# Optimization experiments

Hardware: AMD Instinct MI355X
Metric: run time of the kernel (lower is better)

Reference implementation:

```python
import jax, jax.numpy as jnp
import numpy as np

NUM_EMBEDDINGS = 1024
EMBEDDING_DIM = 64
COMMITMENT_COST = 0.25
N_TOKENS = 131072  # e.g. batch 128 of 32x32 latent grids, flattened


def setup_inputs() -> dict:
    key = jax.random.key(0)
    k1, k2 = jax.random.split(key)
    z_e = jax.random.normal(k1, (N_TOKENS, EMBEDDING_DIM), dtype=jnp.float32)
    # torch init: uniform_(-1/K, 1/K)
    lim = 1.0 / NUM_EMBEDDINGS
    embeddings = jax.random.uniform(
        k2, (NUM_EMBEDDINGS, EMBEDDING_DIM), dtype=jnp.float32,
        minval=-lim, maxval=lim)
    return {"z_e": z_e, "embeddings": embeddings}


def reference(z_e, embeddings):
    # Squared L2 distances via the expanded form: ||z||^2 - 2 z.E^T + ||e||^2.
    # Same math as sum((z[:,None,:]-E[None,:,:])**2, -1) without the (N,K,D)
    # intermediate; only additive constants per-row, so argmin is identical.
    z_sq = jnp.sum(z_e * z_e, axis=1, keepdims=True)           # [N,1]
    e_sq = jnp.sum(embeddings * embeddings, axis=1)            # [K]
    distances = z_sq - 2.0 * (z_e @ embeddings.T) + e_sq[None, :]  # [N,K]
    encoding_indices = jnp.argmin(distances, axis=1)           # [N] int
    z_q = embeddings[encoding_indices]                         # [N,D]

    sg = jax.lax.stop_gradient
    codebook_loss = jnp.mean((sg(z_q) - z_e) ** 2)
    commit_loss = jnp.mean((z_q - sg(z_e)) ** 2)
    vq_loss = codebook_loss + COMMITMENT_COST * commit_loss

    # Straight-through estimator
    z_q_st = z_e + sg(z_q - z_e)
    return z_q_st, vq_loss, encoding_indices
```

## Files before the change

kernel.cpp:

```cpp
#include <hip/hip_runtime.h>

#define NTOK   131072
#define KCODES 1024
#define DIM    64
#define BM     128
#define BN     64
#define NCT    (KCODES / BN)
#define SLOT_CAP 16384

#define LOSS_OFF (NTOK * DIM)
#define IDX_OFF  (LOSS_OFF + 1)

#define EPS_U 6e-5f

typedef __attribute__((ext_vector_type(8))) short bf16x8;
typedef __attribute__((ext_vector_type(4))) float f32x4;
typedef __attribute__((ext_vector_type(4))) unsigned short ush4;

#if defined(__has_builtin)
#if __has_builtin(__builtin_amdgcn_global_load_lds)
#define HAVE_GLD 1
#endif
#endif

#ifdef HAVE_GLD
typedef const __attribute__((address_space(1))) unsigned int* gas_u32p;
typedef __attribute__((address_space(3))) unsigned int* las_u32p;
#define GLD16(ldst, gsrc) \
    __builtin_amdgcn_global_load_lds((gas_u32p)(gsrc), (las_u32p)(ldst), 16, 0, 0)
#endif

__device__ inline unsigned short bf16rtn(float x) {
    unsigned u = __float_as_uint(x);
    return (unsigned short)((u + 0x7fffu + ((u >> 16) & 1u)) >> 16);
}

__device__ inline unsigned long long packdi(float d, int idx) {
    unsigned b = __float_as_uint(d);
    b ^= (b & 0x80000000u) ? 0xFFFFFFFFu : 0x80000000u;
    return ((unsigned long long)b << 32) | (unsigned)idx;
}

__global__ __launch_bounds__(256) void prep_kernel(const float* __restrict__ E,
                                                   unsigned short* __restrict__ Bswz,
                                                   float* __restrict__ esqh,
                                                   float* __restrict__ esq,
                                                   int* __restrict__ cnt) {
    const int t = threadIdx.x, b = blockIdx.x;
    if (b == 0 && t == 0) cnt[0] = 0;
    int id = b * 256 + t;
    int c = id >> 6, k = id & 63;
    float x = E[id];
    unsigned short h = bf16rtn(x);
    float hf = __uint_as_float(((unsigned)h) << 16);
    unsigned short lo = bf16rtn(x - hf);
    int rx = (c & 7) << 4;
    int qh = (k >> 3) << 4;
    int ob = (k & 7) << 1;
    Bswz[(c * 256 + (qh ^ rx) + ob) >> 1]           = h;
    Bswz[(c * 256 + ((128 + qh) ^ rx) + ob) >> 1]   = lo;
    if (b < 4) {
        int cc = b * 256 + t;
        const float4* row = (const float4*)(E + cc * DIM);
        float s = 0.f;
        #pragma unroll
        for (int i = 0; i < DIM / 4; ++i) {
            float4 v = row[i];
            s += v.x * v.x + v.y * v.y + v.z * v.z + v.w * v.w;
        }
        esq[cc] = s;
        esqh[cc] = 0.5f * s;
    }
}

__global__ __launch_bounds__(512, 4) void mfma_argmin_kernel(
    const float* __restrict__ z, const float* __restrict__ E,
    const unsigned short* __restrict__ Bswz, const float* __restrict__ esqh_g,
    float* __restrict__ idx_out, float* __restrict__ out0,
    float* __restrict__ partials, int* __restrict__ cnt, int* __restrict__ wl,
    unsigned long long* __restrict__ bitmap) {
    __shared__ __align__(16) char lds[49152];
    __shared__ __align__(16) char aux[4096];
    float* esqh_s  = (float*)aux;
    float* cb_best = (float*)aux;
    float* cb_sec  = (float*)(aux + 1024);
    int*   cb_idx  = (int*)(aux + 2048);
    int*   fbi     = (int*)(aux + 3072);
    float* wred    = (float*)(aux + 3584);

    const int t = threadIdx.x;
    const int l = t & 63;
    const int w = t >> 6;
    const int rg = w >> 1;
    const int cg = w & 1;
    const int lan15 = l & 15;
    const int kp16 = (l >> 4) * 16;
    const int xr = (lan15 & 7) << 4;
    const int row0 = blockIdx.x * BM;
    const char* gb = (const char*)Bswz;
    const int goff = w * 2048 + l * 16;

#ifdef HAVE_GLD
    GLD16(lds + 32768 + w * 2048,        gb + goff);
    GLD16(lds + 32768 + w * 2048 + 1024, gb + goff + 1024);
#else
    uint4 pv0a = *(const uint4*)(gb + goff);
    uint4 pv0b = *(const uint4*)(gb + goff + 1024);
#endif

    esqh_s[t]       = esqh_g[t];
    esqh_s[512 + t] = esqh_g[512 + t];

    {
        const float4* zg = (const float4*)(z + (size_t)row0 * DIM);
        float4 av[4];
        #pragma unroll
        for (int p = 0; p < 4; ++p) av[p] = zg[p * 512 + t];
        #pragma unroll
        for (int p = 0; p < 4; ++p) {
            int li = p * 512 + t;
            int r = li >> 4, q = li & 15;
            float xs[4] = {av[p].x, av[p].y, av[p].z, av[p].w};
            ush4 hv, lv;
            #pragma unroll
            for (int j = 0; j < 4; ++j) {
                unsigned short h = bf16rtn(xs[j]);
                float hf = __uint_as_float(((unsigned)h) << 16);
                hv[j] = h;
                lv[j] = bf16rtn(xs[j] - hf);
            }
            int rxw = (r & 7) << 4;
            int o = ((q * 8) ^ rxw);
            *(ush4*)(lds + r * 128 + o)         = hv;
            *(ush4*)(lds + 16384 + r * 128 + o) = lv;
        }
    }
#ifndef HAVE_GLD
    *(uint4*)(lds + 32768 + goff)        = pv0a;
    *(uint4*)(lds + 32768 + goff + 1024) = pv0b;
#endif
    __syncthreads();

    const int ko0 = kp16 ^ xr;
    const int ko1 = (64 + kp16) ^ xr;
    const int arow = (rg * 32 + lan15) * 128;
    const char* alo = lds + 16384 + arow;

    bf16x8 ah00 = *(const bf16x8*)(lds + arow + ko0);
    bf16x8 ah01 = *(const bf16x8*)(lds + arow + ko1);
    bf16x8 ah10 = *(const bf16x8*)(lds + arow + 2048 + ko0);
    bf16x8 ah11 = *(const bf16x8*)(lds + arow + 2048 + ko1);
    __syncthreads();

    float best[8], second[8];
    int   bidx[8];
    #pragma unroll
    for (int s = 0; s < 8; ++s) { best[s] = 3.4e38f; second[s] = 3.4e38f; bidx[s] = 0; }

    const int brow = (cg * 32 + lan15) * 256;

    for (int ct = 0; ct < NCT; ++ct) {
        char* cur = lds + ((ct & 1) ^ 1) * 32768;
        if (ct < NCT - 1) {
            char* nbuf = lds + (ct & 1) * 32768;
            const char* g = gb + (ct + 1) * 16384 + goff;
#ifdef HAVE_GLD
            GLD16(nbuf + w * 2048,        g);
            GLD16(nbuf + w * 2048 + 1024, g + 1024);
#else
            *(uint4*)(nbuf + goff)        = *(const uint4*)(g);
            *(uint4*)(nbuf + goff + 1024) = *(const uint4*)(g + 1024);
#endif
        }

        f32x4 acc[2][2];
        #pragma unroll
        for (int fr = 0; fr < 2; ++fr)
            #pragma unroll
            for (int fc = 0; fc < 2; ++fc)
                acc[fr][fc] = (f32x4){0.f, 0.f, 0.f, 0.f};

        #pragma unroll
        for (int fc = 0; fc < 2; ++fc) {
            const char* bp = cur + brow + fc * 4096;
            bf16x8 b0 = *(const bf16x8*)(bp + ko0);
            bf16x8 b1 = *(const bf16x8*)(bp + ko1);
            acc[0][fc] = __builtin_amdgcn_mfma_f32_16x16x32_bf16(ah00, b0, acc[0][fc], 0, 0, 0);
            acc[1][fc] = __builtin_amdgcn_mfma_f32_16x16x32_bf16(ah10, b0, acc[1][fc], 0, 0, 0);
            acc[0][fc] = __builtin_amdgcn_mfma_f32_16x16x32_bf16(ah01, b1, acc[0][fc], 0, 0, 0);
            acc[1][fc] = __builtin_amdgcn_mfma_f32_16x16x32_bf16(ah11, b1, acc[1][fc], 0, 0, 0);
            {
                bf16x8 al0 = *(const bf16x8*)(alo + ko0);
                bf16x8 al1 = *(const bf16x8*)(alo + 2048 + ko0);
                acc[0][fc] = __builtin_amdgcn_mfma_f32_16x16x32_bf16(al0, b0, acc[0][fc], 0, 0, 0);
                acc[1][fc] = __builtin_amdgcn_mfma_f32_16x16x32_bf16(al1, b0, acc[1][fc], 0, 0, 0);
            }
            {
                bf16x8 al2 = *(const bf16x8*)(alo + ko1);
                bf16x8 al3 = *(const bf16x8*)(alo + 2048 + ko1);
                acc[0][fc] = __builtin_amdgcn_mfma_f32_16x16x32_bf16(al2, b1, acc[0][fc], 0, 0, 0);
                acc[1][fc] = __builtin_amdgcn_mfma_f32_16x16x32_bf16(al3, b1, acc[1][fc], 0, 0, 0);
            }
            {
                bf16x8 b2 = *(const bf16x8*)(bp + 128 + ko0);
                acc[0][fc] = __builtin_amdgcn_mfma_f32_16x16x32_bf16(ah00, b2, acc[0][fc], 0, 0, 0);
                acc[1][fc] = __builtin_amdgcn_mfma_f32_16x16x32_bf16(ah10, b2, acc[1][fc], 0, 0, 0);
            }
            {
                bf16x8 b3 = *(const bf16x8*)(bp + 128 + ko1);
                acc[0][fc] = __builtin_amdgcn_mfma_f32_16x16x32_bf16(ah01, b3, acc[0][fc], 0, 0, 0);
                acc[1][fc] = __builtin_amdgcn_mfma_f32_16x16x32_bf16(ah11, b3, acc[1][fc], 0, 0, 0);
            }
        }

        #pragma unroll
        for (int fc = 0; fc < 2; ++fc) {
            int col = ct * BN + cg * 32 + fc * 16 + lan15;
            float eh = esqh_s[col];
            #pragma unroll
            for (int fr = 0; fr < 2; ++fr) {
                #pragma unroll
                for (int r = 0; r < 4; ++r) {
                    float u = eh - acc[fr][fc][r];
                    int s = fr * 4 + r;
                    second[s] = fminf(second[s], fmaxf(u, best[s]));
                    bidx[s] = (u < best[s]) ? col : bidx[s];
                    best[s] = fminf(u, best[s]);
                }
            }
        }
        __syncthreads();
    }

    #pragma unroll
    for (int s = 0; s < 8; ++s) {
        float b = best[s], sc = second[s];
        int bi = bidx[s];
        #pragma unroll
        for (int off = 1; off <= 8; off <<= 1) {
            float ob = __shfl_xor(b, off);
            float os = __shfl_xor(sc, off);
            int   oi = __shfl_xor(bi, off);
            float mx = fmaxf(b, ob);
            sc = fminf(fminf(sc, os), mx);
            if (ob < b) { b = ob; bi = oi; }
            else if (ob == b) bi = min(bi, oi);
        }
        best[s] = b; second[s] = sc; bidx[s] = bi;
    }
    if (lan15 == 0) {
        #pragma unroll
        for (int s = 0; s < 8; ++s) {
            int row = rg * 32 + (s >> 2) * 16 + (l >> 4) * 4 + (s & 3);
            cb_best[cg * BM + row] = best[s];
            cb_sec [cg * BM + row] = second[s];
            cb_idx [cg * BM + row] = bidx[s];
        }
    }
    __syncthreads();
    if (t < BM) {
        float b0 = cb_best[t], b1 = cb_best[BM + t];
        float s0 = cb_sec[t],  s1 = cb_sec[BM + t];
        int   i0 = cb_idx[t],  i1 = cb_idx[BM + t];
        float b; int bi;
        if (b1 < b0 || (b1 == b0 && i1 < i0)) { b = b1; bi = i1; }
        else                                  { b = b0; bi = i0; }
        float sec = fminf(fminf(s0, s1), fmaxf(b0, b1));
        int gid = row0 + t;
        idx_out[gid] = (float)bi;
        bool flg = (sec - b <= EPS_U);
        fbi[t] = bi | (flg ? 0x80000000 : 0);
        unsigned long long mask = __ballot(flg);
        if (l == 0) bitmap[blockIdx.x * 2 + w] = mask;
        int nf = __popcll(mask);
        int base = 0;
        if (l == 0 && nf) base = atomicAdd(cnt, nf);
        base = __shfl(base, 0);
        if (flg) {
            int pos = __popcll(mask & ((1ull << l) - 1ull));
            int slot = base + pos;
            if (slot < SLOT_CAP) wl[slot] = gid;
        }
    }
    __syncthreads();

    {
        const int tk = t >> 2, qd = t & 3;
        int pk = fbi[tk];
        int bi = pk & 0x3FF;
        bool fl = pk < 0;
        const float4* zr = (const float4*)z + (size_t)(row0 + tk) * 16 + qd * 4;
        const float4* er = (const float4*)E + (size_t)bi * 16 + qd * 4;
        float4* orow = (float4*)out0 + (size_t)(row0 + tk) * 16 + qd * 4;
        float ls = 0.f;
        #pragma unroll
        for (int j = 0; j < 4; ++j) {
            float4 zv = zr[j], ev = er[j];
            float dx = ev.x - zv.x, dy = ev.y - zv.y;
            float dz = ev.z - zv.z, dw = ev.w - zv.w;
            float4 o = {zv.x + dx, zv.y + dy, zv.z + dz, zv.w + dw};
            orow[j] = o;
            ls += dx * dx + dy * dy + dz * dz + dw * dw;
        }
        if (fl) ls = 0.f;
        #pragma unroll
        for (int off = 1; off <= 32; off <<= 1) ls += __shfl_xor(ls, off);
        if (l == 0) wred[w] = ls;
    }
    __syncthreads();
    if (t == 0) {
        float s = 0.f;
        #pragma unroll
        for (int i = 0; i < 8; ++i) s += wred[i];
        partials[blockIdx.x] = s;
    }
}

__global__ __launch_bounds__(256) void fallback_kernel(
    const float* __restrict__ z, const float* __restrict__ E,
    const float* __restrict__ esq_g, unsigned long long* __restrict__ cand,
    const int* __restrict__ wl, const int* __restrict__ cnt_p) {
    __shared__ __align__(16) float es[DIM][128];
    __shared__ __align__(16) float zl[16][72];
    __shared__ float zqs[16];

    const int t = threadIdx.x;
    const int tg = t >> 4;
    const int cs = t & 15;
    const int cnt = min(*cnt_p, SLOT_CAP);
    const int nwork = ((cnt + 15) >> 4) << 2;

    for (int cb = blockIdx.x; cb < nwork; cb += 2048) {
        const int chunk = cb >> 2, qtr = cb & 3;
        const int base = chunk * 16;
        const int nval = min(16, cnt - base);
        const int tok = wl[base + (tg < nval ? tg : 0)];
        {
            float4 v = ((const float4*)z)[(size_t)tok * 16 + cs];
            *(float4*)&zl[tg][cs * 4] = v;
        }
        __syncthreads();
        if (t < 16) {
            float s = 0.f;
            for (int k = 0; k < DIM; ++k) { float v = zl[t][k]; s += v * v; }
            zqs[t] = s;
        }
        __syncthreads();
        const float zq = zqs[tg];

        float best = 3.4e38f;
        int bi = 0;
        for (int ti = 0; ti < 2; ++ti) {
            const int tile = qtr * 2 + ti;
            const float4* eg = (const float4*)(E + (size_t)tile * 128 * DIM);
            #pragma unroll
            for (int p = 0; p < 8; ++p) {
                int li = p * 256 + t;
                int c = li & 127, k4 = li >> 7;
                float4 v = eg[c * 16 + k4];
                es[k4 * 4 + 0][c] = v.x;
                es[k4 * 4 + 1][c] = v.y;
                es[k4 * 4 + 2][c] = v.z;
                es[k4 * 4 + 3][c] = v.w;
            }
            __syncthreads();

            float acc[8];
            #pragma unroll
            for (int n = 0; n < 8; ++n) acc[n] = 0.f;
            #pragma unroll 8
            for (int k = 0; k < DIM; ++k) {
                float a = zl[tg][k];
                float4 b0 = *(const float4*)&es[k][cs * 8 + 0];
                float4 b1 = *(const float4*)&es[k][cs * 8 + 4];
                float b[8] = {b0.x, b0.y, b0.z, b0.w, b1.x, b1.y, b1.z, b1.w};
                #pragma unroll
                for (int n = 0; n < 8; ++n) acc[n] += a * b[n];
            }
            #pragma unroll
            for (int n = 0; n < 8; ++n) {
                int c = tile * 128 + cs * 8 + n;
                float d = (zq - 2.0f * acc[n]) + esq_g[c];
                if (d < best) { best = d; bi = c; }
            }
            __syncthreads();
        }
        #pragma unroll
        for (int off = 1; off <= 8; off <<= 1) {
            float ob = __shfl_xor(best, off);
            int   oi = __shfl_xor(bi, off);
            if (ob < best || (ob == best && oi < bi)) { best = ob; bi = oi; }
        }
        if (cs == 0 && tg < nval)
            cand[(size_t)(base + tg) * 4 + qtr] = packdi(best, bi);
        __syncthreads();
    }
}

__global__ __launch_bounds__(256) void repair_kernel(
    const float* __restrict__ z, const float* __restrict__ E,
    float* __restrict__ idx_out, float* __restrict__ out0,
    float* __restrict__ contrib, const unsigned long long* __restrict__ cand,
    const int* __restrict__ wl, const int* __restrict__ cnt_p) {
    const int t = threadIdx.x;
    const int tg = t >> 4;
    const int cs = t & 15;
    const int cnt = min(*cnt_p, SLOT_CAP);

    for (int s0 = blockIdx.x * 16; s0 < cnt; s0 += 512 * 16) {
        int s = s0 + tg;
        if (s < cnt) {
            int tok = wl[s];
            unsigned long long m = cand[(size_t)s * 4 + 0];
            m = min(m, cand[(size_t)s * 4 + 1]);
            m = min(m, cand[(size_t)s * 4 + 2]);
            m = min(m, cand[(size_t)s * 4 + 3]);
            int bi = (int)(unsigned)(m & 0xFFFFFFFFull);
            float4 zv = ((const float4*)z)[(size_t)tok * 16 + cs];
            float4 ev = ((const float4*)E)[(size_t)bi * 16 + cs];
            float dx = ev.x - zv.x, dy = ev.y - zv.y;
            float dz = ev.z - zv.z, dw = ev.w - zv.w;
            float4 o = {zv.x + dx, zv.y + dy, zv.z + dz, zv.w + dw};
            ((float4*)out0)[(size_t)tok * 16 + cs] = o;
            float c4 = dx * dx + dy * dy + dz * dz + dw * dw;
            #pragma unroll
            for (int off = 1; off <= 8; off <<= 1) c4 += __shfl_xor(c4, off);
            if (cs == 0) {
                idx_out[tok] = (float)bi;
                contrib[tok] = c4;
            }
        }
    }
}

__global__ __launch_bounds__(256) void loss_kernel(
    const float* __restrict__ partials, const unsigned long long* __restrict__ bitmap,
    const float* __restrict__ contrib, float* __restrict__ loss_out) {
    __shared__ float red[256];
    const int t = threadIdx.x;
    float p = 0.f;
    #pragma unroll
    for (int i = 0; i < 4; ++i) p += partials[t * 4 + i];
    for (int wi = t * 8; wi < t * 8 + 8; ++wi) {
        unsigned long long m = bitmap[wi];
        while (m) {
            int b = __builtin_ctzll(m);
            p += contrib[wi * 64 + b];
            m &= m - 1;
        }
    }
    red[t] = p;
    __syncthreads();
    for (int s = 128; s >= 1; s >>= 1) {
        if (t < s) red[t] += red[t + s];
        __syncthreads();
    }
    if (t == 0) {
        float m = red[0] / (float)(NTOK * DIM);
        loss_out[0] = m + 0.25f * m;
    }
}

extern "C" void kernel_launch(void* const* d_in, const int* in_sizes, int n_in,
                              void* d_out, int out_size, void* d_ws, size_t ws_size,
                              hipStream_t stream) {
    const float* z = (const float*)d_in[0];
    const float* E = (const float*)d_in[1];
    float* out = (float*)d_out;

    char* wsb = (char*)d_ws;
    float*              esq      = (float*)(wsb);
    float*              esqh     = (float*)(wsb + 4096);
    float*              partials = (float*)(wsb + 8192);
    int*                cnt      = (int*)(wsb + 16384);
    int*                wl       = (int*)(wsb + 20480);
    unsigned long long* bitmap   = (unsigned long long*)(wsb + 86016);
    unsigned short*     Bswz     = (unsigned short*)(wsb + 102400);
    float*              contrib  = (float*)(wsb + 364544);
    unsigned long long* cand     = (unsigned long long*)(wsb + 888832);

    prep_kernel<<<256, 256, 0, stream>>>(E, Bswz, esqh, esq, cnt);
    mfma_argmin_kernel<<<NTOK / BM, 512, 0, stream>>>(z, E, Bswz, esqh,
                                                      out + IDX_OFF, out,
                                                      partials, cnt, wl, bitmap);
    fallback_kernel<<<2048, 256, 0, stream>>>(z, E, esq, cand, wl, cnt);
    repair_kernel<<<512, 256, 0, stream>>>(z, E, out + IDX_OFF, out, contrib,
                                           cand, wl, cnt);
    loss_kernel<<<1, 256, 0, stream>>>(partials, bitmap, contrib, out + LOSS_OFF);
}
```

Measured before the change: 145.5 us.

## Double codebook tile width and hoist low-part A fragments into registers

Widens the codebook tile per iteration from 64 to 128 codes, halving the number of loop iterations and barriers, and grows LDS from 48KB to 64KB. Each wave now computes four 16-column fragments. The bf16 low-part A fragments are loaded once into registers before the loop instead of being re-read from LDS every tile. The margin threshold EPS_U is halved, which changes how many rows go to the exact fallback path. The trade-off is higher register and LDS pressure, which may reduce occupancy, and a tighter epsilon whose correctness depends on the precision margin.

```diff
diff --git a/kernel.cpp b/kernel.cpp
--- a/kernel.cpp
+++ b/kernel.cpp
@@ -4,14 +4,14 @@
 #define KCODES 1024
 #define DIM    64
 #define BM     128
-#define BN     64
+#define BN     128
 #define NCT    (KCODES / BN)
 #define SLOT_CAP 16384
 
 #define LOSS_OFF (NTOK * DIM)
 #define IDX_OFF  (LOSS_OFF + 1)
 
-#define EPS_U 6e-5f
+#define EPS_U 3e-5f
 
 typedef __attribute__((ext_vector_type(8))) short bf16x8;
 typedef __attribute__((ext_vector_type(4))) float f32x4;
@@ -79,7 +79,7 @@
     float* __restrict__ idx_out, float* __restrict__ out0,
     float* __restrict__ partials, int* __restrict__ cnt, int* __restrict__ wl,
     unsigned long long* __restrict__ bitmap) {
-    __shared__ __align__(16) char lds[49152];
+    __shared__ __align__(16) char lds[65536];
     __shared__ __align__(16) char aux[4096];
     float* esqh_s  = (float*)aux;
     float* cb_best = (float*)aux;
@@ -98,14 +98,16 @@
     const int xr = (lan15 & 7) << 4;
     const int row0 = blockIdx.x * BM;
     const char* gb = (const char*)Bswz;
-    const int goff = w * 2048 + l * 16;
 
 #ifdef HAVE_GLD
-    GLD16(lds + 32768 + w * 2048,        gb + goff);
-    GLD16(lds + 32768 + w * 2048 + 1024, gb + goff + 1024);
+    #pragma unroll
+    for (int p = 0; p < 4; ++p)
+        GLD16(lds + 32768 + p * 8192 + t * 16, gb + p * 8192 + t * 16);
 #else
-    uint4 pv0a = *(const uint4*)(gb + goff);
-    uint4 pv0b = *(const uint4*)(gb + goff + 1024);
+    uint4 pv0[4];
+    #pragma unroll
+    for (int p = 0; p < 4; ++p)
+        pv0[p] = *(const uint4*)(gb + p * 8192 + t * 16);
 #endif
 
     esqh_s[t]       = esqh_g[t];
@@ -136,20 +138,24 @@
         }
     }
 #ifndef HAVE_GLD
-    *(uint4*)(lds + 32768 + goff)        = pv0a;
-    *(uint4*)(lds + 32768 + goff + 1024) = pv0b;
+    #pragma unroll
+    for (int p = 0; p < 4; ++p)
+        *(uint4*)(lds + 32768 + p * 8192 + t * 16) = pv0[p];
 #endif
     __syncthreads();
 
     const int ko0 = kp16 ^ xr;
     const int ko1 = (64 + kp16) ^ xr;
     const int arow = (rg * 32 + lan15) * 128;
-    const char* alo = lds + 16384 + arow;
 
     bf16x8 ah00 = *(const bf16x8*)(lds + arow + ko0);
     bf16x8 ah01 = *(const bf16x8*)(lds + arow + ko1);
     bf16x8 ah10 = *(const bf16x8*)(lds + arow + 2048 + ko0);
     bf16x8 ah11 = *(const bf16x8*)(lds + arow + 2048 + ko1);
+    bf16x8 al00 = *(const bf16x8*)(lds + 16384 + arow + ko0);
+    bf16x8 al01 = *(const bf16x8*)(lds + 16384 + arow + ko1);
+    bf16x8 al10 = *(const bf16x8*)(lds + 16384 + arow + 2048 + ko0);
+    bf16x8 al11 = *(const bf16x8*)(lds + 16384 + arow + 2048 + ko1);
     __syncthreads();
 
     float best[8], second[8];
@@ -157,31 +163,34 @@
     #pragma unroll
     for (int s = 0; s < 8; ++s) { best[s] = 3.4e38f; second[s] = 3.4e38f; bidx[s] = 0; }
 
-    const int brow = (cg * 32 + lan15) * 256;
+    const int brow = (cg * 64 + lan15) * 256;
 
     for (int ct = 0; ct < NCT; ++ct) {
         char* cur = lds + ((ct & 1) ^ 1) * 32768;
         if (ct < NCT - 1) {
             char* nbuf = lds + (ct & 1) * 32768;
-            const char* g = gb + (ct + 1) * 16384 + goff;
+            const char* g = gb + (size_t)(ct + 1) * 32768;
 #ifdef HAVE_GLD
-            GLD16(nbuf + w * 2048,        g);
-            GLD16(nbuf + w * 2048 + 1024, g + 1024);
+            #pragma unroll
+            for (int p = 0; p < 4; ++p)
+                GLD16(nbuf + p * 8192 + t * 16, g + p * 8192 + t * 16);
 #else
-            *(uint4*)(nbuf + goff)        = *(const uint4*)(g);
-            *(uint4*)(nbuf + goff + 1024) = *(const uint4*)(g + 1024);
-#endif
-        }
-
-        f32x4 acc[2][2];
+            #pragma unroll
+            for (int p = 0; p < 4; ++p)
+                *(uint4*)(nbuf + p * 8192 + t * 16) =
+                    *(const uint4*)(g + p * 8192 + t * 16);
+#endif
+        }
+
+        f32x4 acc[2][4];
         #pragma unroll
         for (int fr = 0; fr < 2; ++fr)
             #pragma unroll
-            for (int fc = 0; fc < 2; ++fc)
+            for (int fc = 0; fc < 4; ++fc)
                 acc[fr][fc] = (f32x4){0.f, 0.f, 0.f, 0.f};
 
         #pragma unroll
-        for (int fc = 0; fc < 2; ++fc) {
+        for (int fc = 0; fc < 4; ++fc) {
             const char* bp = cur + brow + fc * 4096;
             bf16x8 b0 = *(const bf16x8*)(bp + ko0);
             bf16x8 b1 = *(const bf16x8*)(bp + ko1);
@@ -189,18 +198,10 @@
             acc[1][fc] = __builtin_amdgcn_mfma_f32_16x16x32_bf16(ah10, b0, acc[1][fc], 0, 0, 0);
             acc[0][fc] = __builtin_amdgcn_mfma_f32_16x16x32_bf16(ah01, b1, acc[0][fc], 0, 0, 0);
             acc[1][fc] = __builtin_amdgcn_mfma_f32_16x16x32_bf16(ah11, b1, acc[1][fc], 0, 0, 0);
-            {
-                bf16x8 al0 = *(const bf16x8*)(alo + ko0);
-                bf16x8 al1 = *(const bf16x8*)(alo + 2048 + ko0);
-                acc[0][fc] = __builtin_amdgcn_mfma_f32_16x16x32_bf16(al0, b0, acc[0][fc], 0, 0, 0);
-                acc[1][fc] = __builtin_amdgcn_mfma_f32_16x16x32_bf16(al1, b0, acc[1][fc], 0, 0, 0);
-            }
-            {
-                bf16x8 al2 = *(const bf16x8*)(alo + ko1);
-                bf16x8 al3 = *(const bf16x8*)(alo + 2048 + ko1);
-                acc[0][fc] = __builtin_amdgcn_mfma_f32_16x16x32_bf16(al2, b1, acc[0][fc], 0, 0, 0);
-                acc[1][fc] = __builtin_amdgcn_mfma_f32_16x16x32_bf16(al3, b1, acc[1][fc], 0, 0, 0);
-            }
+            acc[0][fc] = __builtin_amdgcn_mfma_f32_16x16x32_bf16(al00, b0, acc[0][fc], 0, 0, 0);
+            acc[1][fc] = __builtin_amdgcn_mfma_f32_16x16x32_bf16(al10, b0, acc[1][fc], 0, 0, 0);
+            acc[0][fc] = __builtin_amdgcn_mfma_f32_16x16x32_bf16(al01, b1, acc[0][fc], 0, 0, 0);
+            acc[1][fc] = __builtin_amdgcn_mfma_f32_16x16x32_bf16(al11, b1, acc[1][fc], 0, 0, 0);
             {
                 bf16x8 b2 = *(const bf16x8*)(bp + 128 + ko0);
                 acc[0][fc] = __builtin_amdgcn_mfma_f32_16x16x32_bf16(ah00, b2, acc[0][fc], 0, 0, 0);
@@ -214,8 +215,8 @@
         }
 
         #pragma unroll
-        for (int fc = 0; fc < 2; ++fc) {
-            int col = ct * BN + cg * 32 + fc * 16 + lan15;
+        for (int fc = 0; fc < 4; ++fc) {
+            int col = ct * BN + cg * 64 + fc * 16 + lan15;
             float eh = esqh_s[col];
             #pragma unroll
             for (int fr = 0; fr < 2; ++fr) {
```

After: 120.0 us (median of 2 runs). -17.5%, faster.
